# Kernel optimization log

Measured on AMD Instinct MI355X. Metric: run time of the kernel, lower is better.

## Reference

```python
import jax, jax.numpy as jnp
import numpy as np

B, T, D, U = 64, 512, 512, 1024


def setup_inputs() -> dict:
    key = jax.random.key(0)
    k1, k2, k3 = jax.random.split(key, 3)
    x = jax.random.normal(k1, (B, T, D), dtype=jnp.float32)
    kernel = jax.random.normal(k2, (D, 4 * U), dtype=jnp.float32) * (1.0 / np.sqrt(D))
    rec_kernel = jax.random.normal(k3, (U, 4 * U), dtype=jnp.float32) * (1.0 / np.sqrt(U))
    return {"x": x, "kernel": kernel, "rec_kernel": rec_kernel}


def reference(x, kernel, rec_kernel):
    """SimpleLSTM forward: returns last hidden state h_T of shape [B, U].
    Gate order along the 4U axis is (i, f, c, o), matching the kernel split.
    No biases; initial h and c are zeros (as in the original call()).
    """
    units = rec_kernel.shape[0]
    # Precompute input contributions for all timesteps in one big GEMM:
    # x_gates[b, t, :] == x[b, t] @ kernel  (same math as 4 per-gate matmuls)
    x_gates = jnp.einsum('btd,dk->tbk', x, kernel)  # [T, B, 4U]

    def step(carry, xt):
        h, c = carry
        z = xt + h @ rec_kernel  # [B, 4U]
        i = jax.nn.sigmoid(z[:, :units])
        f = jax.nn.sigmoid(z[:, units:2 * units])
        g = jnp.tanh(z[:, 2 * units:3 * units])
        o = jax.nn.sigmoid(z[:, 3 * units:])
        c_new = f * c + i * g
        h_new = o * jnp.tanh(c_new)
        return (h_new, c_new), None

    batch = x.shape[0]
    h0 = jnp.zeros((batch, units), dtype=x.dtype)
    c0 = jnp.zeros((batch, units), dtype=x.dtype)
    (h_last, _), _ = jax.lax.scan(step, (h0, c0), x_gates)
    return h_last
```

## Files before the change

### kernel.cpp

```cpp
#include <hip/hip_runtime.h>
#include <stdint.h>

#define WS_XB   0LL
#define WS_H    33554432LL
#define WS_FLAG 33816576LL

typedef unsigned short u16;
typedef unsigned int   u32;
typedef unsigned long long u64;
typedef __attribute__((ext_vector_type(8))) short short8;
typedef __attribute__((ext_vector_type(4))) float f32x4;

__device__ __forceinline__ u16 f2bf(float f) {
  unsigned u = __float_as_uint(f);
  u += 0x7FFFu + ((u >> 16) & 1u);
  return (u16)(u >> 16);
}
__device__ __forceinline__ float fast_tanh(float x) {
  float e = __expf(2.f * x);
  return 1.f - 2.f / (e + 1.f);
}

__global__ void conv_x(const float* __restrict__ x, u16* __restrict__ xb) {
  long gid = (long)blockIdx.x * blockDim.x + threadIdx.x;
  long sr = gid >> 6;
  int  d0 = (int)(gid & 63) * 8;
  int  b = (int)(sr >> 9), t = (int)(sr & 511);
  const float* src = x + sr * 512 + d0;
  float4 v0 = *(const float4*)(src);
  float4 v1 = *(const float4*)(src + 4);
  u16 tmp[8] = {f2bf(v0.x), f2bf(v0.y), f2bf(v0.z), f2bf(v0.w),
                f2bf(v1.x), f2bf(v1.y), f2bf(v1.z), f2bf(v1.w)};
  *(short8*)(xb + ((long)t * 64 + b) * 512 + d0) = *(short8*)tmp;
}

__launch_bounds__(256, 1)
__global__ void lstm_fused(const float* __restrict__ kern, const float* __restrict__ rec,
                           const u16* __restrict__ xb, u32* __restrict__ hbuf,
                           u32* __restrict__ flags, float* __restrict__ out) {
  __shared__ u16   smH[2][32 * 64 * 8];
  __shared__ float zscr[4][16][20];

  const int bid = blockIdx.x;
  const int bg = bid >> 6;
  const int ut = bid & 63;
  const int tid = threadIdx.x;
  const int w = tid >> 6, lane = tid & 63;
  const int quad = lane >> 4, n15 = lane & 15;
  const int gate = n15 >> 2, uu = n15 & 3;
  const int rowE = quad * 4 + gate;

  short8 wf[48];
  const size_t gcol = (size_t)gate * 1024 + (size_t)ut * 16 + (size_t)(w * 4 + uu);
#pragma unroll
  for (int ks = 0; ks < 32; ++ks) {
    u16 tmp[8];
#pragma unroll
    for (int j = 0; j < 8; ++j)
      tmp[j] = f2bf(rec[(size_t)(ks * 32 + quad * 8 + j) * 4096 + gcol]);
    wf[ks] = *(short8*)tmp;
  }
#pragma unroll
  for (int ks = 0; ks < 16; ++ks) {
    u16 tmp[8];
#pragma unroll
    for (int j = 0; j < 8; ++j)
      tmp[j] = f2bf(kern[(size_t)(ks * 32 + quad * 8 + j) * 4096 + gcol]);
    wf[32 + ks] = *(short8*)tmp;
  }

  float c = 0.f;

#pragma unroll
  for (int j = 0; j < 8; ++j)
    *(uint4*)(&smH[0][(tid + j * 256) * 8]) = (uint4){0u, 0u, 0u, 0u};

  short8 xf[16];
  {
    const u16* xr = xb + (size_t)(bg * 16 + n15) * 512 + quad * 8;
#pragma unroll
    for (int ks = 0; ks < 16; ++ks) xf[ks] = *(const short8*)(xr + ks * 32);
  }
  f32x4 acc0 = {0.f, 0.f, 0.f, 0.f}, acc1 = {0.f, 0.f, 0.f, 0.f};
#pragma unroll
  for (int ks = 0; ks < 16; ks += 2) {
    acc0 = __builtin_amdgcn_mfma_f32_16x16x32_bf16(xf[ks], wf[32 + ks], acc0, 0, 0, 0);
    acc1 = __builtin_amdgcn_mfma_f32_16x16x32_bf16(xf[ks + 1], wf[33 + ks], acc1, 0, 0, 0);
  }
  __syncthreads();

#define X8_MFMA(S)                                                                 \
  _Pragma("unroll")                                                                \
  for (int ks2 = (S); ks2 < (S) + 8; ks2 += 2) {                                   \
    acc0 = __builtin_amdgcn_mfma_f32_16x16x32_bf16(xf[ks2], wf[32 + ks2], acc0, 0, 0, 0);     \
    acc1 = __builtin_amdgcn_mfma_f32_16x16x32_bf16(xf[ks2 + 1], wf[33 + ks2], acc1, 0, 0, 0); \
  }

#define PAYLOAD_LOAD                                                               \
  {                                                                                \
    const u32* hs = hbuf + (size_t)pb * 32768 + (size_t)(bg * 16 + n15) * 512 + quad * 4; \
    _Pragma("unroll")                                                              \
    for (int kk = 0; kk < 8; ++kk) {                                               \
      const u64* src = (const u64*)(hs + (w * 8 + kk) * 16);                       \
      pay[2 * kk]     = __hip_atomic_load(src,     __ATOMIC_RELAXED, __HIP_MEMORY_SCOPE_AGENT); \
      pay[2 * kk + 1] = __hip_atomic_load(src + 1, __ATOMIC_RELAXED, __HIP_MEMORY_SCOPE_AGENT); \
    }                                                                              \
  }

#define OWN8(BASE)                                                                 \
  _Pragma("unroll")                                                                \
  for (int kk = 0; kk < 8; ++kk) {                                                 \
    union { u64 q[2]; short8 s; u32 d[4]; } uo;                                    \
    uo.q[0] = pay[2 * kk]; uo.q[1] = pay[2 * kk + 1];                              \
    if (kk & 1) acc1 = __builtin_amdgcn_mfma_f32_16x16x32_bf16(uo.s, wf[(BASE) + kk], acc1, 0, 0, 0); \
    else        acc0 = __builtin_amdgcn_mfma_f32_16x16x32_bf16(uo.s, wf[(BASE) + kk], acc0, 0, 0, 0); \
    *(uint4*)(smH[pb] + (((BASE) + kk) * 64 + lane) * 8) =                         \
        (uint4){uo.d[0], uo.d[1], uo.d[2], uo.d[3]};                               \
  }

  for (int t = 0; t < 512; ++t) {
    __builtin_amdgcn_s_setprio(1);
    const u16* sh = smH[t & 1];
#pragma unroll
    for (int g = 0; g < 4; ++g) {
      if (g == w) continue;
#pragma unroll
      for (int kk = 0; kk < 8; kk += 2) {
        const int ks = g * 8 + kk;
        short8 a0 = *(const short8*)(sh + (ks * 64 + lane) * 8);
        acc0 = __builtin_amdgcn_mfma_f32_16x16x32_bf16(a0, wf[ks], acc0, 0, 0, 0);
        short8 a1 = *(const short8*)(sh + ((ks + 1) * 64 + lane) * 8);
        acc1 = __builtin_amdgcn_mfma_f32_16x16x32_bf16(a1, wf[ks + 1], acc1, 0, 0, 0);
      }
    }
    __builtin_amdgcn_s_setprio(0);

    const int cw = uu * 4 + gate;
    zscr[w][quad * 4 + 0][cw] = acc0[0] + acc1[0];
    zscr[w][quad * 4 + 1][cw] = acc0[1] + acc1[1];
    zscr[w][quad * 4 + 2][cw] = acc0[2] + acc1[2];
    zscr[w][quad * 4 + 3][cw] = acc0[3] + acc1[3];
    asm volatile("s_waitcnt lgkmcnt(0)" ::: "memory");
    __builtin_amdgcn_sched_barrier(0);
    float4 zv = *(const float4*)&zscr[w][rowE][uu * 4];

    float ig = 1.f / (1.f + __expf(-zv.x));
    float fg = 1.f / (1.f + __expf(-zv.y));
    float gg = fast_tanh(zv.z);
    float og = 1.f / (1.f + __expf(-zv.w));
    c = fg * c + ig * gg;
    float h = og * fast_tanh(c);

    if (t == 511) {
      out[(size_t)(bg * 16 + rowE) * 1024 + (size_t)(ut * 16 + w * 4 + uu)] = h;
      break;
    }

    const int pb = (t + 1) & 1;

    {
      u16 hu = f2bf(h);
      int other = __shfl_xor((int)(unsigned)hu, 1);
      if ((uu & 1) == 0) {
        u32 pw = (u32)hu | ((u32)(unsigned)other << 16);
        __hip_atomic_store(&hbuf[(size_t)pb * 32768 + (size_t)(bg * 16 + rowE) * 512
                                 + ut * 8 + w * 2 + (uu >> 1)],
                           pw, __ATOMIC_RELAXED, __HIP_MEMORY_SCOPE_AGENT);
      }
    }
    __builtin_amdgcn_sched_barrier(0);

    {
      const u16* xr = xb + ((size_t)(t + 1) * 64 + bg * 16 + n15) * 512 + quad * 8;
#pragma unroll
      for (int ks2 = 0; ks2 < 16; ++ks2) xf[ks2] = *(const short8*)(xr + ks2 * 32);
    }
    __builtin_amdgcn_sched_barrier(0);

    asm volatile("s_waitcnt vmcnt(16)" ::: "memory");
    asm volatile("s_barrier" ::: "memory");
    if (tid == 0)
      __hip_atomic_store(&flags[(bg * 64 + ut) * 32], (u32)(t + 1),
                         __ATOMIC_RELAXED, __HIP_MEMORY_SCOPE_AGENT);

    acc0 = (f32x4){0.f, 0.f, 0.f, 0.f};
    acc1 = (f32x4){0.f, 0.f, 0.f, 0.f};

    u64 pay[16];
    if (w == 0) {
      const u32 tgt = (u32)(t + 1);
      const u32* fp = &flags[(bg * 64 + lane) * 32];
      u32 v = __hip_atomic_load(fp, __ATOMIC_RELAXED, __HIP_MEMORY_SCOPE_AGENT);
      while (__ballot(v < tgt) != 0ull) {
        v = __hip_atomic_load(fp, __ATOMIC_RELAXED, __HIP_MEMORY_SCOPE_AGENT);
      }
      __builtin_amdgcn_s_setprio(1);
      PAYLOAD_LOAD;
    } else {
      __builtin_amdgcn_s_setprio(1);
      X8_MFMA(0);
    }
    asm volatile("s_barrier" ::: "memory");
    if (w == 0) {
      X8_MFMA(0);
      X8_MFMA(8);
    } else {
      PAYLOAD_LOAD;
      X8_MFMA(8);
    }

    if      (w == 0) { OWN8(0)  }
    else if (w == 1) { OWN8(8)  }
    else if (w == 2) { OWN8(16) }
    else             { OWN8(24) }
    __builtin_amdgcn_s_setprio(0);

    asm volatile("s_waitcnt lgkmcnt(0)" ::: "memory");
    asm volatile("s_barrier" ::: "memory");
  }
}

extern "C" void kernel_launch(void* const* d_in, const int* in_sizes, int n_in,
                              void* d_out, int out_size, void* d_ws, size_t ws_size,
                              hipStream_t stream) {
  const float* x    = (const float*)d_in[0];
  const float* kern = (const float*)d_in[1];
  const float* rec  = (const float*)d_in[2];
  float* out = (float*)d_out;
  char* ws = (char*)d_ws;

  u16* xbp   = (u16*)(ws + WS_XB);
  u32* hbuf  = (u32*)(ws + WS_H);
  u32* flags = (u32*)(ws + WS_FLAG);

  hipMemsetAsync(ws + WS_FLAG, 0, 32768, stream);

  conv_x<<<8192, 256, 0, stream>>>(x, xbp);

  lstm_fused<<<256, 256, 0, stream>>>(kern, rec, xbp, hbuf, flags, out);
}
```

Before: 2.940 ms.

## Merge unit tiles into 512-thread blocks to halve grid and flag polling

Each workgroup now has 8 waves covering 32 hidden units instead of 4 waves covering 16, so the grid drops from 256 to 128 blocks. Each block polls 32 peer flags instead of 64, and the h-slice loads and LDS staging are split into four k-slices per wave. The intent is to cut the cost of cross-block synchronisation per timestep. In exchange only half as many compute units are used, each SIMD carries twice the MFMA work, and the 512-thread, 2-block launch bound caps per-wave registers, which could force the large weight-fragment array to spill.

Measured after the change: 8.801 ms. +199.4%, slower.

```diff
diff --git a/kernel.cpp b/kernel.cpp
--- a/kernel.cpp
+++ b/kernel.cpp
@@ -34,16 +34,16 @@
   *(short8*)(xb + ((long)t * 64 + b) * 512 + d0) = *(short8*)tmp;
 }
 
-__launch_bounds__(256, 1)
+__launch_bounds__(512, 2)
 __global__ void lstm_fused(const float* __restrict__ kern, const float* __restrict__ rec,
                            const u16* __restrict__ xb, u32* __restrict__ hbuf,
                            u32* __restrict__ flags, float* __restrict__ out) {
   __shared__ u16   smH[2][32 * 64 * 8];
-  __shared__ float zscr[4][16][20];
+  __shared__ float zscr[8][16][20];
 
   const int bid = blockIdx.x;
-  const int bg = bid >> 6;
-  const int ut = bid & 63;
+  const int bg = bid >> 5;
+  const int ut2 = bid & 31;
   const int tid = threadIdx.x;
   const int w = tid >> 6, lane = tid & 63;
   const int quad = lane >> 4, n15 = lane & 15;
@@ -51,7 +51,7 @@
   const int rowE = quad * 4 + gate;
 
   short8 wf[48];
-  const size_t gcol = (size_t)gate * 1024 + (size_t)ut * 16 + (size_t)(w * 4 + uu);
+  const size_t gcol = (size_t)gate * 1024 + (size_t)ut2 * 32 + (size_t)(w * 4 + uu);
 #pragma unroll
   for (int ks = 0; ks < 32; ++ks) {
     u16 tmp[8];
@@ -72,8 +72,8 @@
   float c = 0.f;
 
 #pragma unroll
-  for (int j = 0; j < 8; ++j)
-    *(uint4*)(&smH[0][(tid + j * 256) * 8]) = (uint4){0u, 0u, 0u, 0u};
+  for (int j = 0; j < 4; ++j)
+    *(uint4*)(&smH[0][(tid + j * 512) * 8]) = (uint4){0u, 0u, 0u, 0u};
 
   short8 xf[16];
   {
@@ -96,25 +96,25 @@
     acc1 = __builtin_amdgcn_mfma_f32_16x16x32_bf16(xf[ks2 + 1], wf[33 + ks2], acc1, 0, 0, 0); \
   }
 
-#define PAYLOAD_LOAD                                                               \
+#define PAYLOAD4                                                                   \
   {                                                                                \
     const u32* hs = hbuf + (size_t)pb * 32768 + (size_t)(bg * 16 + n15) * 512 + quad * 4; \
     _Pragma("unroll")                                                              \
-    for (int kk = 0; kk < 8; ++kk) {                                               \
-      const u64* src = (const u64*)(hs + (w * 8 + kk) * 16);                       \
+    for (int kk = 0; kk < 4; ++kk) {                                               \
+      const u64* src = (const u64*)(hs + (w * 4 + kk) * 16);                       \
       pay[2 * kk]     = __hip_atomic_load(src,     __ATOMIC_RELAXED, __HIP_MEMORY_SCOPE_AGENT); \
       pay[2 * kk + 1] = __hip_atomic_load(src + 1, __ATOMIC_RELAXED, __HIP_MEMORY_SCOPE_AGENT); \
     }                                                                              \
   }
 
-#define OWN8(BASE)                                                                 \
+#define OWN4                                                                       \
   _Pragma("unroll")                                                                \
-  for (int kk = 0; kk < 8; ++kk) {                                                 \
+  for (int kk = 0; kk < 4; ++kk) {                                                 \
     union { u64 q[2]; short8 s; u32 d[4]; } uo;                                    \
     uo.q[0] = pay[2 * kk]; uo.q[1] = pay[2 * kk + 1];                              \
-    if (kk & 1) acc1 = __builtin_amdgcn_mfma_f32_16x16x32_bf16(uo.s, wf[(BASE) + kk], acc1, 0, 0, 0); \
-    else        acc0 = __builtin_amdgcn_mfma_f32_16x16x32_bf16(uo.s, wf[(BASE) + kk], acc0, 0, 0, 0); \
-    *(uint4*)(smH[pb] + (((BASE) + kk) * 64 + lane) * 8) =                         \
+    if (kk & 1) acc1 = __builtin_amdgcn_mfma_f32_16x16x32_bf16(uo.s, wf[w * 4 + kk], acc1, 0, 0, 0); \
+    else        acc0 = __builtin_amdgcn_mfma_f32_16x16x32_bf16(uo.s, wf[w * 4 + kk], acc0, 0, 0, 0); \
+    *(uint4*)(smH[pb] + ((w * 4 + kk) * 64 + lane) * 8) =                          \
         (uint4){uo.d[0], uo.d[1], uo.d[2], uo.d[3]};                               \
   }
 
@@ -122,11 +122,11 @@
     __builtin_amdgcn_s_setprio(1);
     const u16* sh = smH[t & 1];
 #pragma unroll
-    for (int g = 0; g < 4; ++g) {
+    for (int g = 0; g < 8; ++g) {
       if (g == w) continue;
 #pragma unroll
-      for (int kk = 0; kk < 8; kk += 2) {
-        const int ks = g * 8 + kk;
+      for (int kk = 0; kk < 4; kk += 2) {
+        const int ks = g * 4 + kk;
         short8 a0 = *(const short8*)(sh + (ks * 64 + lane) * 8);
         acc0 = __builtin_amdgcn_mfma_f32_16x16x32_bf16(a0, wf[ks], acc0, 0, 0, 0);
         short8 a1 = *(const short8*)(sh + ((ks + 1) * 64 + lane) * 8);
@@ -152,7 +152,7 @@
     float h = og * fast_tanh(c);
 
     if (t == 511) {
-      out[(size_t)(bg * 16 + rowE) * 1024 + (size_t)(ut * 16 + w * 4 + uu)] = h;
+      out[(size_t)(bg * 16 + rowE) * 1024 + (size_t)(ut2 * 32 + w * 4 + uu)] = h;
       break;
     }
 
@@ -164,7 +164,7 @@
       if ((uu & 1) == 0) {
         u32 pw = (u32)hu | ((u32)(unsigned)other << 16);
         __hip_atomic_store(&hbuf[(size_t)pb * 32768 + (size_t)(bg * 16 + rowE) * 512
-                                 + ut * 8 + w * 2 + (uu >> 1)],
+                                 + ut2 * 16 + w * 2 + (uu >> 1)],
                            pw, __ATOMIC_RELAXED, __HIP_MEMORY_SCOPE_AGENT);
       }
     }
@@ -180,22 +180,22 @@
     asm volatile("s_waitcnt vmcnt(16)" ::: "memory");
     asm volatile("s_barrier" ::: "memory");
     if (tid == 0)
-      __hip_atomic_store(&flags[(bg * 64 + ut) * 32], (u32)(t + 1),
+      __hip_atomic_store(&flags[(bg * 32 + ut2) * 32], (u32)(t + 1),
                          __ATOMIC_RELAXED, __HIP_MEMORY_SCOPE_AGENT);
 
     acc0 = (f32x4){0.f, 0.f, 0.f, 0.f};
     acc1 = (f32x4){0.f, 0.f, 0.f, 0.f};
 
-    u64 pay[16];
+    u64 pay[8];
     if (w == 0) {
       const u32 tgt = (u32)(t + 1);
-      const u32* fp = &flags[(bg * 64 + lane) * 32];
+      const u32* fp = &flags[(bg * 32 + (lane & 31)) * 32];
       u32 v = __hip_atomic_load(fp, __ATOMIC_RELAXED, __HIP_MEMORY_SCOPE_AGENT);
       while (__ballot(v < tgt) != 0ull) {
         v = __hip_atomic_load(fp, __ATOMIC_RELAXED, __HIP_MEMORY_SCOPE_AGENT);
       }
       __builtin_amdgcn_s_setprio(1);
-      PAYLOAD_LOAD;
+      PAYLOAD4;
     } else {
       __builtin_amdgcn_s_setprio(1);
       X8_MFMA(0);
@@ -205,14 +205,11 @@
       X8_MFMA(0);
       X8_MFMA(8);
     } else {
-      PAYLOAD_LOAD;
+      PAYLOAD4;
       X8_MFMA(8);
     }
 
-    if      (w == 0) { OWN8(0)  }
-    else if (w == 1) { OWN8(8)  }
-    else if (w == 2) { OWN8(16) }
-    else             { OWN8(24) }
+    OWN4;
     __builtin_amdgcn_s_setprio(0);
 
     asm volatile("s_waitcnt lgkmcnt(0)" ::: "memory");
@@ -237,5 +234,5 @@
 
   conv_x<<<8192, 256, 0, stream>>>(x, xbp);
 
-  lstm_fused<<<256, 256, 0, stream>>>(kern, rec, xbp, hbuf, flags, out);
-}
+  lstm_fused<<<128, 512, 0, stream>>>(kern, rec, xbp, hbuf, flags, out);
+}
```
